# Kernel optimization log

Measured on AMD Instinct MI355X. Metric: run time of the kernel, lower is better.

## Reference

```python
import jax, jax.numpy as jnp
import numpy as np

B, N, D, L, T = 64, 64, 128, 4, 10  # batch, atoms, hidden_dim, n_layers, n_atom_types
EPS = 1e-5


def setup_inputs() -> dict:
    key = jax.random.key(0)
    ks = jax.random.split(key, 10)
    def rn(k, shape, s=0.05):
        return jax.random.normal(k, shape, jnp.float32) * s
    return dict(
        positions=jax.random.normal(ks[0], (B, N, 3), jnp.float32),
        atomic_numbers=jax.random.randint(ks[1], (B, N), 0, T),
        embed=rn(ks[2], (T, D)),
        edge_w1=rn(ks[3], (L, 2 * D + 1, D)), edge_b1=jnp.zeros((L, D), jnp.float32),
        edge_w2=rn(ks[4], (L, D, D)), edge_b2=jnp.zeros((L, D), jnp.float32),
        node_w1=rn(ks[5], (L, 2 * D, D)), node_b1=jnp.zeros((L, D), jnp.float32),
        node_w2=rn(ks[6], (L, D, D)), node_b2=jnp.zeros((L, D), jnp.float32),
        ln_g=jnp.ones((L, D), jnp.float32), ln_b=jnp.zeros((L, D), jnp.float32),
        out_w=rn(ks[7], (D, 3)), out_b=jnp.zeros((3,), jnp.float32),
    )


def _layer(h, dist_sq, ew1, eb1, ew2, eb2, nw1, nb1, nw2, nb2, g, b):
    # edge_mlp first linear on cat([h_i, h_j, dist_sq]) == h@Wa (bcast over j)
    # + h@Wb (bcast over i) + dist_sq * w_d, avoiding materializing the concat.
    wa, wb, wd = ew1[:D], ew1[D:2 * D], ew1[2 * D]
    pre = (h @ wa)[:, :, None, :] + (h @ wb)[:, None, :, :] + dist_sq * wd + eb1  # [B,N,N,D]
    m_ij = jax.nn.silu(jax.nn.silu(pre) @ ew2 + eb2)
    m_i = m_ij.mean(axis=2)  # mean over j -> [B,N,D]
    # node_mlp on cat([h, m_i]) split the same way; dropout is eval-mode identity.
    h_out = jax.nn.silu(h @ nw1[:D] + m_i @ nw1[D:] + nb1) @ nw2 + nb2
    x = h + h_out
    mu = x.mean(-1, keepdims=True)
    var = ((x - mu) ** 2).mean(-1, keepdims=True)
    return (x - mu) / jnp.sqrt(var + EPS) * g + b


def reference(positions, atomic_numbers, embed, edge_w1, edge_b1, edge_w2, edge_b2,
              node_w1, node_b1, node_w2, node_b2, ln_g, ln_b, out_w, out_b):
    h = embed[atomic_numbers]  # [B,N,D]
    diff = positions[:, :, None, :] - positions[:, None, :, :]
    dist_sq = (diff ** 2).sum(-1, keepdims=True)  # [B,N,N,1]
    for i in range(L):
        h = _layer(h, dist_sq, edge_w1[i], edge_b1[i], edge_w2[i], edge_b2[i],
                   node_w1[i], node_b1[i], node_w2[i], node_b2[i], ln_g[i], ln_b[i])
    return h @ out_w + out_b  # [B,N,3]
```

## Files before the change

kernel.cpp:

```cpp
#include <hip/hip_runtime.h>


typedef _Float16 f16;
typedef _Float16 f16x4 __attribute__((ext_vector_type(4)));
typedef _Float16 f16x8 __attribute__((ext_vector_type(8)));
typedef float f32x4 __attribute__((ext_vector_type(4)));

__device__ __forceinline__ float bf2f(unsigned short u) {
    union { unsigned int i; float f; } v; v.i = ((unsigned int)u) << 16; return v.f;
}
__device__ __forceinline__ unsigned short f2bf(float f) {
    union { float f; unsigned int i; } v; v.f = f;
    unsigned int x = v.i;
    return (unsigned short)((x + 0x7fffu + ((x >> 16) & 1u)) >> 16);
}
__device__ __forceinline__ float silu_f(float x) {
    float e = __builtin_amdgcn_exp2f(-1.44269504088896f * x);
    return x * __builtin_amdgcn_rcpf(1.0f + e);
}

struct Ptrs { const void* p[14]; };

__device__ __forceinline__ float ldf(const void* p, int i, int bf) {
    return bf ? bf2f(((const unsigned short*)p)[i]) : ((const float*)p)[i];
}

#define SWZ_TOTAL 393216
#define SMALL_TOTAL 17539

__global__ __launch_bounds__(256) void prep_kernel(
    Ptrs ptrs, f16* dst, float* sc)
{
    __shared__ int flgsh;
    int t = threadIdx.x;
    if (t < 64) {
        int ex = (((const unsigned short*)ptrs.p[0])[t * 2] >> 7) & 0xFF;
        unsigned long long m = __ballot(ex >= 110 && ex <= 135);
        if (t == 0) flgsh = (__popcll(m) >= 40) ? 1 : 0;
    }
    __syncthreads();
    int bf = flgsh;

    int gid = blockIdx.x * 256 + t;
    if (gid < SWZ_TOTAL) {
        int lay = gid / 98304;
        int r   = gid % 98304;
        const void* src; int base, rowoff = 0, r2;
        if (r < 49152) {
            int mat = r >> 14; r2 = r & 16383;
            if (mat == 0)      { src = ptrs.p[2]; base = lay * 32896; }
            else if (mat == 1) { src = ptrs.p[2]; base = lay * 32896; rowoff = 128; }
            else               { src = ptrs.p[4]; base = lay * 16384; }
        } else if (r < 81920) {
            r2 = r - 49152; src = ptrs.p[6]; base = lay * 32768;
        } else {
            r2 = r - 81920; src = ptrs.p[8]; base = lay * 16384;
        }
        int s = r2 >> 12, q = r2 & 4095;
        int j = q & 7, l = (q >> 3) & 63, c = q >> 9;
        int row = rowoff + s * 32 + ((l >> 4) << 3) + j;
        int col = (c << 4) + (l & 15);
        dst[gid] = (f16)ldf(src, base + row * 128 + col, bf);
    } else {
        int sid = gid - SWZ_TOTAL;
        if (sid >= SMALL_TOTAL) return;
        const void* src; int i;
        if      (sid < 12288) { src = ptrs.p[0]; i = sid; }
        else if (sid < 13568) { src = ptrs.p[1]; i = sid - 12288; }
        else if (sid < 14080) { int k = sid - 13568;
                                src = ptrs.p[2]; i = (k >> 7) * 32896 + 32768 + (k & 127); }
        else if (sid < 14592) { src = ptrs.p[3];  i = sid - 14080; }
        else if (sid < 15104) { src = ptrs.p[5];  i = sid - 14592; }
        else if (sid < 15616) { src = ptrs.p[7];  i = sid - 15104; }
        else if (sid < 16128) { src = ptrs.p[9];  i = sid - 15616; }
        else if (sid < 16640) { src = ptrs.p[10]; i = sid - 16128; }
        else if (sid < 17152) { src = ptrs.p[11]; i = sid - 16640; }
        else if (sid < 17536) { src = ptrs.p[12]; i = sid - 17152; }
        else                  { src = ptrs.p[13]; i = sid - 17536; }
        sc[sid] = ldf(src, i, bf);
    }
}

__global__ __launch_bounds__(256) void embed_ab_kernel(
    const int* an, const float* sc, const f16* wa, const f16* wb,
    const float* eb1C, f16* h16, f16* a16, f16* b16)
{
    int t = threadIdx.x;
    int w = t >> 6, lane = t & 63;
    int row0 = blockIdx.x << 4;
    int m_ = lane & 15, q_ = lane >> 4;
    const float* emb = sc + 12288;
    int a = an[row0 + m_];
    a = a < 0 ? 0 : (a > 9 ? 9 : a);
    f16x8 afrag[4];
#pragma unroll
    for (int s = 0; s < 4; s++) {
        f32x4 u0 = *(const f32x4*)(emb + a * 128 + s * 32 + q_ * 8);
        f32x4 u1 = *(const f32x4*)(emb + a * 128 + s * 32 + q_ * 8 + 4);
        f16x8 hv;
#pragma unroll
        for (int e = 0; e < 4; e++) { hv[e] = (f16)u0[e]; hv[e + 4] = (f16)u1[e]; }
        afrag[s] = hv;
        if (w == 0)
            *(f16x8*)(h16 + (row0 + m_) * 128 + s * 32 + q_ * 8) = hv;
    }
#pragma unroll
    for (int mat = 0; mat < 2; mat++) {
        const f16* W = mat ? wb : wa;
        f16* out     = mat ? b16 : a16;
#pragma unroll
        for (int cc = 0; cc < 2; cc++) {
            int c = 2 * w + cc;
            float init = mat ? 0.0f : eb1C[c * 16 + m_];
            f32x4 acc = { init, init, init, init };
#pragma unroll
            for (int s = 0; s < 4; s++) {
                f16x8 bfr = *(const f16x8*)(W + ((s * 8 + c) * 64 + lane) * 8);
                acc = __builtin_amdgcn_mfma_f32_16x16x32_f16(afrag[s], bfr, acc, 0, 0, 0);
            }
#pragma unroll
            for (int r = 0; r < 4; r++)
                out[(row0 + q_ * 4 + r) * 128 + c * 16 + m_] = (f16)acc[r];
        }
    }
}

__global__ __launch_bounds__(256) void edge_kernel(
    const float* sc, const f16* a16, const f16* b16,
    const f16* ew2_swz, const float* eb2C, const float* wdC, f16* m_out)
{
    __shared__ f16 Wlds[8192];
    __shared__ f16 S[64 * 136];
    __shared__ float a_sh[128];
    __shared__ float wd_sh[128];
    __shared__ float dsq_sh[64];

    int t  = threadIdx.x;
    int ig = blockIdx.x;
    int b  = ig >> 6;
    const float* posC = sc;

#pragma unroll
    for (int k = 0; k < 4; k++) {
        int idx = (k * 256 + t) * 8;
        *(f16x8*)(Wlds + idx) = *(const f16x8*)(ew2_swz + idx);
    }
    if (t < 128) a_sh[t] = (float)a16[ig * 128 + t];
    else         wd_sh[t - 128] = wdC[t - 128];
    if (t < 64) {
        float xi = posC[ig * 3 + 0], yi = posC[ig * 3 + 1], zi = posC[ig * 3 + 2];
        int jg = b * 64 + t;
        float dx = xi - posC[jg * 3 + 0];
        float dy = yi - posC[jg * 3 + 1];
        float dz = zi - posC[jg * 3 + 2];
        dsq_sh[t] = dx * dx + dy * dy + dz * dz;
    }
    __syncthreads();

    {
        int dj = t >> 5;
        int dbase = (t & 31) * 4;
#pragma unroll
        for (int p = 0; p < 8; p++) {
            int j = p * 8 + dj;
            f16x4 bv = *(const f16x4*)(b16 + (b * 64 + j) * 128 + dbase);
            float ds = dsq_sh[j];
            float p0 = a_sh[dbase + 0] + (float)bv[0] + ds * wd_sh[dbase + 0];
            float p1 = a_sh[dbase + 1] + (float)bv[1] + ds * wd_sh[dbase + 1];
            float p2 = a_sh[dbase + 2] + (float)bv[2] + ds * wd_sh[dbase + 2];
            float p3 = a_sh[dbase + 3] + (float)bv[3] + ds * wd_sh[dbase + 3];
            f16x4 sv = { (f16)silu_f(p0), (f16)silu_f(p1),
                         (f16)silu_f(p2), (f16)silu_f(p3) };
            *(f16x4*)(S + j * 136 + dbase) = sv;
        }
    }
    __syncthreads();

    int lane = t & 63, w = t >> 6;
    int m_ = lane & 15, q_ = lane >> 4;
    f32x4 acc[8];
#pragma unroll
    for (int c = 0; c < 8; c++) {
        float e = eb2C[c * 16 + m_];
        acc[c] = (f32x4){ e, e, e, e };
    }
#pragma unroll
    for (int s = 0; s < 2; s++) {
        f16x8 af = *(const f16x8*)(S + (w * 16 + m_) * 136 + s * 32 + q_ * 8);
#pragma unroll
        for (int c = 0; c < 8; c++) {
            f16x8 bfr = *(const f16x8*)(Wlds + ((s * 8 + c) * 64 + lane) * 8);
            acc[c] = __builtin_amdgcn_mfma_f32_16x16x32_f16(af, bfr, acc[c], 0, 0, 0);
        }
    }
    __syncthreads();
#pragma unroll
    for (int k = 0; k < 4; k++) {
        int idx = (k * 256 + t) * 8;
        *(f16x8*)(Wlds + idx) = *(const f16x8*)(ew2_swz + 8192 + idx);
    }
    __syncthreads();
#pragma unroll
    for (int s = 2; s < 4; s++) {
        f16x8 af = *(const f16x8*)(S + (w * 16 + m_) * 136 + s * 32 + q_ * 8);
#pragma unroll
        for (int c = 0; c < 8; c++) {
            f16x8 bfr = *(const f16x8*)(Wlds + (((s - 2) * 8 + c) * 64 + lane) * 8);
            acc[c] = __builtin_amdgcn_mfma_f32_16x16x32_f16(af, bfr, acc[c], 0, 0, 0);
        }
    }
    float scv8[8];
#pragma unroll
    for (int c = 0; c < 8; c++) {
        float scv = silu_f(acc[c][0]) + silu_f(acc[c][1]) +
                    silu_f(acc[c][2]) + silu_f(acc[c][3]);
        scv += __shfl_xor(scv, 16);
        scv += __shfl_xor(scv, 32);
        scv8[c] = scv;
    }
    __syncthreads();
    float* msum = (float*)S;
    if (lane < 16) {
#pragma unroll
        for (int c = 0; c < 8; c++)
            msum[w * 128 + c * 16 + lane] = scv8[c];
    }
    __syncthreads();
    if (t < 128) {
        float mv = (msum[0 * 128 + t] + msum[1 * 128 + t] +
                    msum[2 * 128 + t] + msum[3 * 128 + t]) * (1.0f / 64.0f);
        m_out[ig * 128 + t] = (f16)mv;
    }
}

__global__ __launch_bounds__(256) void node_mid_kernel(
    const f16* h16, const f16* m16, const f16* nw1s, const f16* nw2s,
    const float* nb1C, const float* nb2C, const float* lngC, const float* lnbC,
    const f16* waN, const f16* wbN, const float* eb1N,
    f16* a16, f16* b16)
{
    __shared__ f16 relay[16 * 136];
    __shared__ float s1sh[4][16], s2sh[4][16];
    int t = threadIdx.x;
    int w = t >> 6, lane = t & 63;
    int row0 = blockIdx.x << 4;
    int m_ = lane & 15, q_ = lane >> 4;

    f16x8 af[8];
#pragma unroll
    for (int s = 0; s < 4; s++) {
        af[s]     = *(const f16x8*)(h16 + (row0 + m_) * 128 + s * 32 + q_ * 8);
        af[s + 4] = *(const f16x8*)(m16 + (row0 + m_) * 128 + s * 32 + q_ * 8);
    }
#pragma unroll
    for (int cc = 0; cc < 2; cc++) {
        int c = 2 * w + cc;
        float e = nb1C[c * 16 + m_];
        f32x4 acc = { e, e, e, e };
#pragma unroll
        for (int s = 0; s < 8; s++) {
            f16x8 bfr = *(const f16x8*)(nw1s + ((s * 8 + c) * 64 + lane) * 8);
            acc = __builtin_amdgcn_mfma_f32_16x16x32_f16(af[s], bfr, acc, 0, 0, 0);
        }
#pragma unroll
        for (int r = 0; r < 4; r++)
            relay[(q_ * 4 + r) * 136 + c * 16 + m_] = (f16)silu_f(acc[r]);
    }
    __syncthreads();
    f16x8 uf[4];
#pragma unroll
    for (int s = 0; s < 4; s++)
        uf[s] = *(const f16x8*)(relay + m_ * 136 + s * 32 + q_ * 8);
    float x[2][4];
#pragma unroll
    for (int cc = 0; cc < 2; cc++) {
        int c = 2 * w + cc;
        float e = nb2C[c * 16 + m_];
        f32x4 acc = { e, e, e, e };
#pragma unroll
        for (int s = 0; s < 4; s++) {
            f16x8 bfr = *(const f16x8*)(nw2s + ((s * 8 + c) * 64 + lane) * 8);
            acc = __builtin_amdgcn_mfma_f32_16x16x32_f16(uf[s], bfr, acc, 0, 0, 0);
        }
#pragma unroll
        for (int r = 0; r < 4; r++)
            x[cc][r] = acc[r] + (float)h16[(row0 + q_ * 4 + r) * 128 + c * 16 + m_];
    }
    float s1p[4], s2p[4];
#pragma unroll
    for (int r = 0; r < 4; r++) {
        s1p[r] = x[0][r] + x[1][r];
        s2p[r] = x[0][r] * x[0][r] + x[1][r] * x[1][r];
    }
#pragma unroll
    for (int msk = 1; msk < 16; msk <<= 1)
#pragma unroll
        for (int r = 0; r < 4; r++) {
            s1p[r] += __shfl_xor(s1p[r], msk);
            s2p[r] += __shfl_xor(s2p[r], msk);
        }
    if (m_ == 0)
#pragma unroll
        for (int r = 0; r < 4; r++) {
            s1sh[w][q_ * 4 + r] = s1p[r];
            s2sh[w][q_ * 4 + r] = s2p[r];
        }
    __syncthreads();
    float mu[4], rs[4];
#pragma unroll
    for (int r = 0; r < 4; r++) {
        int row = q_ * 4 + r;
        float S1 = s1sh[0][row] + s1sh[1][row] + s1sh[2][row] + s1sh[3][row];
        float S2 = s2sh[0][row] + s2sh[1][row] + s2sh[2][row] + s2sh[3][row];
        mu[r] = S1 * (1.0f / 128.0f);
        float var = S2 * (1.0f / 128.0f) - mu[r] * mu[r];
        rs[r] = rsqrtf(var + 1e-5f);
    }
#pragma unroll
    for (int cc = 0; cc < 2; cc++) {
        int c = 2 * w + cc;
#pragma unroll
        for (int r = 0; r < 4; r++) {
            int col = c * 16 + m_;
            int row = row0 + q_ * 4 + r;
            float y = (x[cc][r] - mu[r]) * rs[r] * lngC[col] + lnbC[col];
            ((f16*)h16)[row * 128 + col] = (f16)y;
            relay[(q_ * 4 + r) * 136 + col] = (f16)y;
        }
    }
    __syncthreads();
    f16x8 hf[4];
#pragma unroll
    for (int s = 0; s < 4; s++)
        hf[s] = *(const f16x8*)(relay + m_ * 136 + s * 32 + q_ * 8);
#pragma unroll
    for (int mat = 0; mat < 2; mat++) {
        const f16* W = mat ? wbN : waN;
        f16* out     = mat ? b16 : a16;
#pragma unroll
        for (int cc = 0; cc < 2; cc++) {
            int c = 2 * w + cc;
            float init = mat ? 0.0f : eb1N[c * 16 + m_];
            f32x4 acc = { init, init, init, init };
#pragma unroll
            for (int s = 0; s < 4; s++) {
                f16x8 bfr = *(const f16x8*)(W + ((s * 8 + c) * 64 + lane) * 8);
                acc = __builtin_amdgcn_mfma_f32_16x16x32_f16(hf[s], bfr, acc, 0, 0, 0);
            }
#pragma unroll
            for (int r = 0; r < 4; r++)
                out[(row0 + q_ * 4 + r) * 128 + c * 16 + m_] = (f16)acc[r];
        }
    }
}

__global__ __launch_bounds__(256) void node_final_kernel(
    const void* pos_raw, const f16* h16, const f16* m16,
    const f16* nw1s, const f16* nw2s,
    const float* nb1C, const float* nb2C, const float* lngC, const float* lnbC,
    const float* owC, const float* obC, void* out)
{
    __shared__ f16 relay[16 * 136];
    __shared__ float s1sh[4][16], s2sh[4][16];
    __shared__ float psh[4][16][3];
    __shared__ int flgsh;
    int t = threadIdx.x;
    int w = t >> 6, lane = t & 63;
    int row0 = blockIdx.x << 4;
    int m_ = lane & 15, q_ = lane >> 4;

    if (t < 64) {
        int ex = (((const unsigned short*)pos_raw)[t * 2] >> 7) & 0xFF;
        unsigned long long mk = __ballot(ex >= 110 && ex <= 135);
        if (t == 0) flgsh = (__popcll(mk) >= 40) ? 1 : 0;
    }

    f16x8 af[8];
#pragma unroll
    for (int s = 0; s < 4; s++) {
        af[s]     = *(const f16x8*)(h16 + (row0 + m_) * 128 + s * 32 + q_ * 8);
        af[s + 4] = *(const f16x8*)(m16 + (row0 + m_) * 128 + s * 32 + q_ * 8);
    }
#pragma unroll
    for (int cc = 0; cc < 2; cc++) {
        int c = 2 * w + cc;
        float e = nb1C[c * 16 + m_];
        f32x4 acc = { e, e, e, e };
#pragma unroll
        for (int s = 0; s < 8; s++) {
            f16x8 bfr = *(const f16x8*)(nw1s + ((s * 8 + c) * 64 + lane) * 8);
            acc = __builtin_amdgcn_mfma_f32_16x16x32_f16(af[s], bfr, acc, 0, 0, 0);
        }
#pragma unroll
        for (int r = 0; r < 4; r++)
            relay[(q_ * 4 + r) * 136 + c * 16 + m_] = (f16)silu_f(acc[r]);
    }
    __syncthreads();
    f16x8 uf[4];
#pragma unroll
    for (int s = 0; s < 4; s++)
        uf[s] = *(const f16x8*)(relay + m_ * 136 + s * 32 + q_ * 8);
    float x[2][4];
#pragma unroll
    for (int cc = 0; cc < 2; cc++) {
        int c = 2 * w + cc;
        float e = nb2C[c * 16 + m_];
        f32x4 acc = { e, e, e, e };
#pragma unroll
        for (int s = 0; s < 4; s++) {
            f16x8 bfr = *(const f16x8*)(nw2s + ((s * 8 + c) * 64 + lane) * 8);
            acc = __builtin_amdgcn_mfma_f32_16x16x32_f16(uf[s], bfr, acc, 0, 0, 0);
        }
#pragma unroll
        for (int r = 0; r < 4; r++)
            x[cc][r] = acc[r] + (float)h16[(row0 + q_ * 4 + r) * 128 + c * 16 + m_];
    }
    float s1p[4], s2p[4];
#pragma unroll
    for (int r = 0; r < 4; r++) {
        s1p[r] = x[0][r] + x[1][r];
        s2p[r] = x[0][r] * x[0][r] + x[1][r] * x[1][r];
    }
#pragma unroll
    for (int msk = 1; msk < 16; msk <<= 1)
#pragma unroll
        for (int r = 0; r < 4; r++) {
            s1p[r] += __shfl_xor(s1p[r], msk);
            s2p[r] += __shfl_xor(s2p[r], msk);
        }
    if (m_ == 0)
#pragma unroll
        for (int r = 0; r < 4; r++) {
            s1sh[w][q_ * 4 + r] = s1p[r];
            s2sh[w][q_ * 4 + r] = s2p[r];
        }
    __syncthreads();
    float p[3][4];
#pragma unroll
    for (int r = 0; r < 4; r++) {
        int row = q_ * 4 + r;
        float S1 = s1sh[0][row] + s1sh[1][row] + s1sh[2][row] + s1sh[3][row];
        float S2 = s2sh[0][row] + s2sh[1][row] + s2sh[2][row] + s2sh[3][row];
        float mu = S1 * (1.0f / 128.0f);
        float var = S2 * (1.0f / 128.0f) - mu * mu;
        float rs = rsqrtf(var + 1e-5f);
        float p0 = 0.0f, p1 = 0.0f, p2 = 0.0f;
#pragma unroll
        for (int cc = 0; cc < 2; cc++) {
            int col = (2 * w + cc) * 16 + m_;
            float y = (x[cc][r] - mu) * rs * lngC[col] + lnbC[col];
            p0 += y * owC[col * 3 + 0];
            p1 += y * owC[col * 3 + 1];
            p2 += y * owC[col * 3 + 2];
        }
        p[0][r] = p0; p[1][r] = p1; p[2][r] = p2;
    }
#pragma unroll
    for (int msk = 1; msk < 16; msk <<= 1)
#pragma unroll
        for (int k = 0; k < 3; k++)
#pragma unroll
            for (int r = 0; r < 4; r++)
                p[k][r] += __shfl_xor(p[k][r], msk);
    if (m_ == 0)
#pragma unroll
        for (int r = 0; r < 4; r++)
#pragma unroll
            for (int k = 0; k < 3; k++)
                psh[w][q_ * 4 + r][k] = p[k][r];
    __syncthreads();
    if (t < 16) {
        int row = row0 + t;
        int bf = flgsh;
#pragma unroll
        for (int k = 0; k < 3; k++) {
            float v = psh[0][t][k] + psh[1][t][k] + psh[2][t][k] + psh[3][t][k]
                      + obC[k];
            if (bf) ((unsigned short*)out)[row * 3 + k] = f2bf(v);
            else    ((float*)out)[row * 3 + k] = v;
        }
    }
}

extern "C" void kernel_launch(void* const* d_in, const int* in_sizes, int n_in,
                              void* d_out, int out_size, void* d_ws, size_t ws_size,
                              hipStream_t stream)
{
    const int* an = (const int*)d_in[1];

    char* ws = (char*)d_ws;
    float* sc   = (float*)(ws + 1024);
    f16*   Wswz = (f16*)(ws + (128u << 10));
    f16*   h16  = (f16*)(ws + (1u << 20));
    f16*   a16  = (f16*)(ws + (2u << 20));
    f16*   b16  = (f16*)(ws + (3u << 20));
    f16*   m16  = (f16*)(ws + (4u << 20));

    Ptrs ptrs;
    const int src_idx[14] = {0, 2, 3, 4, 5, 6, 7, 8, 9, 10, 11, 12, 13, 14};
    for (int k = 0; k < 14; k++) ptrs.p[k] = d_in[src_idx[k]];

    prep_kernel<<<1605, 256, 0, stream>>>(ptrs, Wswz, sc);
    embed_ab_kernel<<<256, 256, 0, stream>>>(an, sc, Wswz, Wswz + 16384,
                                             sc + 14080, h16, a16, b16);
    for (int lay = 0; lay < 4; lay++) {
        const f16* wl = Wswz + lay * 98304;
        const float* wdC  = sc + 13568 + lay * 128;
        const float* eb2C = sc + 14592 + lay * 128;
        const float* nb1C = sc + 15104 + lay * 128;
        const float* nb2C = sc + 15616 + lay * 128;
        const float* lngC = sc + 16128 + lay * 128;
        const float* lnbC = sc + 16640 + lay * 128;

        edge_kernel<<<4096, 256, 0, stream>>>(sc, a16, b16, wl + 32768,
                                              eb2C, wdC, m16);
        if (lay < 3) {
            const f16* wlN = Wswz + (lay + 1) * 98304;
            node_mid_kernel<<<256, 256, 0, stream>>>(
                h16, m16, wl + 49152, wl + 81920, nb1C, nb2C, lngC, lnbC,
                wlN, wlN + 16384, sc + 14080 + (lay + 1) * 128, a16, b16);
        } else {
            node_final_kernel<<<256, 256, 0, stream>>>(
                d_in[0], h16, m16, wl + 49152, wl + 81920,
                nb1C, nb2C, lngC, lnbC,
                sc + 17152, sc + 17536, d_out);
        }
    }
}
```

Before: 227.4 us.

## Compute edge pre-activation SiLU in packed half2 and retile edge MFMA 2x2 per wave

The edge kernel's first-stage elementwise work (a + b + dsq*wd then SiLU) now runs in packed half2 arithmetic with wider 16-byte loads, one j row per four threads. This is meant to halve the VALU instruction count for the exp/rcp-heavy SiLU. The second GEMM's wave tiling changes from 16 rows × all 128 columns to 32 rows × 64 columns. Each wave then loads half as many B fragments from LDS and reuses each across two row blocks, and the final reduction sums over two partials instead of four. Computing the exponent and reciprocal in fp16 lowers accuracy and could overflow for large pre-activations.

After: 220.5 us. -3.0%, faster.

```diff
diff --git a/kernel.cpp b/kernel.cpp
--- a/kernel.cpp
+++ b/kernel.cpp
@@ -1,4 +1,5 @@
 #include <hip/hip_runtime.h>
+#include <hip/hip_fp16.h>
 
 
 typedef _Float16 f16;
@@ -6,6 +7,8 @@
 typedef _Float16 f16x8 __attribute__((ext_vector_type(8)));
 typedef float f32x4 __attribute__((ext_vector_type(4)));
 
+union H2x4 { f16x8 v; __half2 h[4]; };
+
 __device__ __forceinline__ float bf2f(unsigned short u) {
     union { unsigned int i; float f; } v; v.i = ((unsigned int)u) << 16; return v.f;
 }
@@ -17,6 +20,10 @@
 __device__ __forceinline__ float silu_f(float x) {
     float e = __builtin_amdgcn_exp2f(-1.44269504088896f * x);
     return x * __builtin_amdgcn_rcpf(1.0f + e);
+}
+__device__ __forceinline__ __half2 silu_h2(__half2 x, __half2 kf, __half2 one2) {
+    __half2 e = h2exp2(__hmul2(x, kf));
+    return __hmul2(x, h2rcp(__hadd2(one2, e)));
 }
 
 struct Ptrs { const void* p[14]; };
@@ -131,8 +138,7 @@
 {
     __shared__ f16 Wlds[8192];
     __shared__ f16 S[64 * 136];
-    __shared__ float a_sh[128];
-    __shared__ float wd_sh[128];
+    __shared__ __half2 wd2_sh[64];
     __shared__ float dsq_sh[64];
 
     int t  = threadIdx.x;
@@ -145,8 +151,10 @@
         int idx = (k * 256 + t) * 8;
         *(f16x8*)(Wlds + idx) = *(const f16x8*)(ew2_swz + idx);
     }
-    if (t < 128) a_sh[t] = (float)a16[ig * 128 + t];
-    else         wd_sh[t - 128] = wdC[t - 128];
+    if (t >= 64 && t < 128) {
+        int u = t - 64;
+        wd2_sh[u] = __floats2half2_rn(wdC[2 * u], wdC[2 * u + 1]);
+    }
     if (t < 64) {
         float xi = posC[ig * 3 + 0], yi = posC[ig * 3 + 1], zi = posC[ig * 3 + 2];
         int jg = b * 64 + t;
@@ -158,39 +166,56 @@
     __syncthreads();
 
     {
-        int dj = t >> 5;
-        int dbase = (t & 31) * 4;
-#pragma unroll
-        for (int p = 0; p < 8; p++) {
-            int j = p * 8 + dj;
-            f16x4 bv = *(const f16x4*)(b16 + (b * 64 + j) * 128 + dbase);
-            float ds = dsq_sh[j];
-            float p0 = a_sh[dbase + 0] + (float)bv[0] + ds * wd_sh[dbase + 0];
-            float p1 = a_sh[dbase + 1] + (float)bv[1] + ds * wd_sh[dbase + 1];
-            float p2 = a_sh[dbase + 2] + (float)bv[2] + ds * wd_sh[dbase + 2];
-            float p3 = a_sh[dbase + 3] + (float)bv[3] + ds * wd_sh[dbase + 3];
-            f16x4 sv = { (f16)silu_f(p0), (f16)silu_f(p1),
-                         (f16)silu_f(p2), (f16)silu_f(p3) };
-            *(f16x4*)(S + j * 136 + dbase) = sv;
+        int j  = t >> 2;
+        int cb = (t & 3) * 32;
+        float dsf = dsq_sh[j];
+        __half dh = __float2half_rn(dsf);
+        __half2 ds2 = __halves2half2(dh, dh);
+        __half2 kf   = __floats2half2_rn(-1.44269504f, -1.44269504f);
+        __half2 one2 = __floats2half2_rn(1.0f, 1.0f);
+        H2x4 a_r[4], wd_r[4];
+#pragma unroll
+        for (int k = 0; k < 4; k++) {
+            a_r[k].v  = *(const f16x8*)(a16 + ig * 128 + cb + k * 8);
+            wd_r[k].v = *(const f16x8*)((const f16*)wd2_sh + cb + k * 8);
+        }
+#pragma unroll
+        for (int k = 0; k < 4; k++) {
+            H2x4 bv, sv;
+            bv.v = *(const f16x8*)(b16 + (b * 64 + j) * 128 + cb + k * 8);
+#pragma unroll
+            for (int e = 0; e < 4; e++) {
+                __half2 pre = __hfma2(ds2, wd_r[k].h[e],
+                                      __hadd2(a_r[k].h[e], bv.h[e]));
+                sv.h[e] = silu_h2(pre, kf, one2);
+            }
+            *(f16x8*)(S + j * 136 + cb + k * 8) = sv.v;
         }
     }
     __syncthreads();
 
     int lane = t & 63, w = t >> 6;
+    int wr = w & 1, wc = w >> 1;
     int m_ = lane & 15, q_ = lane >> 4;
-    f32x4 acc[8];
-#pragma unroll
-    for (int c = 0; c < 8; c++) {
-        float e = eb2C[c * 16 + m_];
-        acc[c] = (f32x4){ e, e, e, e };
+    f32x4 acc[4][2];
+#pragma unroll
+    for (int c = 0; c < 4; c++) {
+        float e = eb2C[(wc * 4 + c) * 16 + m_];
+        acc[c][0] = (f32x4){ e, e, e, e };
+        acc[c][1] = (f32x4){ e, e, e, e };
     }
 #pragma unroll
     for (int s = 0; s < 2; s++) {
-        f16x8 af = *(const f16x8*)(S + (w * 16 + m_) * 136 + s * 32 + q_ * 8);
-#pragma unroll
-        for (int c = 0; c < 8; c++) {
-            f16x8 bfr = *(const f16x8*)(Wlds + ((s * 8 + c) * 64 + lane) * 8);
-            acc[c] = __builtin_amdgcn_mfma_f32_16x16x32_f16(af, bfr, acc[c], 0, 0, 0);
+        f16x8 bfr[4];
+#pragma unroll
+        for (int c = 0; c < 4; c++)
+            bfr[c] = *(const f16x8*)(Wlds + ((s * 8 + wc * 4 + c) * 64 + lane) * 8);
+#pragma unroll
+        for (int mb = 0; mb < 2; mb++) {
+            f16x8 af = *(const f16x8*)(S + ((wr * 2 + mb) * 16 + m_) * 136 + s * 32 + q_ * 8);
+#pragma unroll
+            for (int c = 0; c < 4; c++)
+                acc[c][mb] = __builtin_amdgcn_mfma_f32_16x16x32_f16(af, bfr[c], acc[c][mb], 0, 0, 0);
         }
     }
     __syncthreads();
@@ -202,33 +227,41 @@
     __syncthreads();
 #pragma unroll
     for (int s = 2; s < 4; s++) {
-        f16x8 af = *(const f16x8*)(S + (w * 16 + m_) * 136 + s * 32 + q_ * 8);
-#pragma unroll
-        for (int c = 0; c < 8; c++) {
-            f16x8 bfr = *(const f16x8*)(Wlds + (((s - 2) * 8 + c) * 64 + lane) * 8);
-            acc[c] = __builtin_amdgcn_mfma_f32_16x16x32_f16(af, bfr, acc[c], 0, 0, 0);
-        }
-    }
-    float scv8[8];
-#pragma unroll
-    for (int c = 0; c < 8; c++) {
-        float scv = silu_f(acc[c][0]) + silu_f(acc[c][1]) +
-                    silu_f(acc[c][2]) + silu_f(acc[c][3]);
+        f16x8 bfr[4];
+#pragma unroll
+        for (int c = 0; c < 4; c++)
+            bfr[c] = *(const f16x8*)(Wlds + (((s - 2) * 8 + wc * 4 + c) * 64 + lane) * 8);
+#pragma unroll
+        for (int mb = 0; mb < 2; mb++) {
+            f16x8 af = *(const f16x8*)(S + ((wr * 2 + mb) * 16 + m_) * 136 + s * 32 + q_ * 8);
+#pragma unroll
+            for (int c = 0; c < 4; c++)
+                acc[c][mb] = __builtin_amdgcn_mfma_f32_16x16x32_f16(af, bfr[c], acc[c][mb], 0, 0, 0);
+        }
+    }
+    float scv4[4];
+#pragma unroll
+    for (int c = 0; c < 4; c++) {
+        float scv = 0.0f;
+#pragma unroll
+        for (int mb = 0; mb < 2; mb++)
+#pragma unroll
+            for (int r = 0; r < 4; r++)
+                scv += silu_f(acc[c][mb][r]);
         scv += __shfl_xor(scv, 16);
         scv += __shfl_xor(scv, 32);
-        scv8[c] = scv;
+        scv4[c] = scv;
     }
     __syncthreads();
     float* msum = (float*)S;
     if (lane < 16) {
 #pragma unroll
-        for (int c = 0; c < 8; c++)
-            msum[w * 128 + c * 16 + lane] = scv8[c];
+        for (int c = 0; c < 4; c++)
+            msum[wr * 128 + (wc * 4 + c) * 16 + lane] = scv4[c];
     }
     __syncthreads();
     if (t < 128) {
-        float mv = (msum[0 * 128 + t] + msum[1 * 128 + t] +
-                    msum[2 * 128 + t] + msum[3 * 128 + t]) * (1.0f / 64.0f);
+        float mv = (msum[t] + msum[128 + t]) * (1.0f / 64.0f);
         m_out[ig * 128 + t] = (f16)mv;
     }
 }
```
